# Optimization experiments

Hardware: AMD Instinct MI355X
Metric: run time of the kernel (lower is better)

The kernel has to match this reference:

```python
import jax, jax.numpy as jnp
import numpy as np

N_TYPES = 4
N_REL = 8
N_HEADS = 8
IN_DIM = 256
N_HID = 128
D_K = N_HID // N_HEADS
N_LAYERS = 2
N_NODES = 100000
N_EDGES = 400000


def setup_inputs() -> dict:
    key = jax.random.key(0)
    ks = jax.random.split(key, 24)
    s = 0.05
    inp = {
        'node_feature': jax.random.normal(ks[0], (N_NODES, IN_DIM), jnp.float32),
        'node_type': jax.random.randint(ks[1], (N_NODES,), 0, N_TYPES),
        'edge_index': jax.random.randint(ks[2], (2, N_EDGES), 0, N_NODES),
        'edge_type': jax.random.randint(ks[3], (N_EDGES,), 0, N_REL),
        # per-type input adapters
        'adapt_w': jax.random.normal(ks[4], (N_TYPES, IN_DIM, N_HID), jnp.float32) * s,
        'adapt_b': jnp.zeros((N_TYPES, N_HID), jnp.float32),
        # HGT conv params, stacked over layers
        'k_w': jax.random.normal(ks[5], (N_LAYERS, N_TYPES, N_HID, N_HID), jnp.float32) * s,
        'k_b': jnp.zeros((N_LAYERS, N_TYPES, N_HID), jnp.float32),
        'q_w': jax.random.normal(ks[6], (N_LAYERS, N_TYPES, N_HID, N_HID), jnp.float32) * s,
        'q_b': jnp.zeros((N_LAYERS, N_TYPES, N_HID), jnp.float32),
        'v_w': jax.random.normal(ks[7], (N_LAYERS, N_TYPES, N_HID, N_HID), jnp.float32) * s,
        'v_b': jnp.zeros((N_LAYERS, N_TYPES, N_HID), jnp.float32),
        'a_w': jax.random.normal(ks[8], (N_LAYERS, N_TYPES, N_HID, N_HID), jnp.float32) * s,
        'a_b': jnp.zeros((N_LAYERS, N_TYPES, N_HID), jnp.float32),
        'rel_pri': jnp.ones((N_LAYERS, N_REL, N_HEADS), jnp.float32),
        'rel_att': jnp.tile(jnp.eye(D_K, dtype=jnp.float32), (N_LAYERS, N_REL, N_HEADS, 1, 1))
                   + jax.random.normal(ks[9], (N_LAYERS, N_REL, N_HEADS, D_K, D_K), jnp.float32) * s,
        'rel_msg': jnp.tile(jnp.eye(D_K, dtype=jnp.float32), (N_LAYERS, N_REL, N_HEADS, 1, 1))
                   + jax.random.normal(ks[10], (N_LAYERS, N_REL, N_HEADS, D_K, D_K), jnp.float32) * s,
        'skip': jnp.ones((N_LAYERS, N_TYPES), jnp.float32),
    }
    return inp


def _per_type_linear(x, w, b, node_type, n_idx):
    # x: [N, din], w: [T, din, dout], b: [T, dout] -> gather row for each node's type
    h_all = jnp.einsum('ni,tio->tno', x, w) + b[:, None, :]  # [T, N, dout]
    return h_all[node_type, n_idx]  # [N, dout]


def _edge_softmax(score, tgt, n):
    # score: [E, H]; softmax over incoming edges of each target node
    m = jax.ops.segment_max(score, tgt, num_segments=n)  # [N, H]
    e = jnp.exp(score - m[tgt])
    z = jax.ops.segment_sum(e, tgt, num_segments=n)
    return e / (z[tgt] + 1e-9)


def _hgt_layer(x, node_type, src, tgt, edge_type,
               kw, kb, qw, qb, vw, vb, aw, ab, pri, att_m, msg_m, skip):
    n = x.shape[0]
    n_idx = jnp.arange(n)
    k = _per_type_linear(x, kw, kb, node_type, n_idx).reshape(n, N_HEADS, D_K)
    q = _per_type_linear(x, qw, qb, node_type, n_idx).reshape(n, N_HEADS, D_K)
    v = _per_type_linear(x, vw, vb, node_type, n_idx).reshape(n, N_HEADS, D_K)
    k_src, v_src, q_tgt = k[src], v[src], q[tgt]  # [E, H, dk]
    # per-relation attention/message transforms, accumulated over small fixed R
    k_rel = jnp.zeros_like(k_src)
    v_rel = jnp.zeros_like(v_src)
    for r in range(N_REL):
        msk = (edge_type == r)[:, None, None]
        k_rel = k_rel + jnp.einsum('ehd,hdf->ehf', jnp.where(msk, k_src, 0.0), att_m[r])
        v_rel = v_rel + jnp.einsum('ehd,hdf->ehf', jnp.where(msk, v_src, 0.0), msg_m[r])
    score = (q_tgt * k_rel).sum(-1) * pri[edge_type] * (1.0 / (D_K ** 0.5))  # [E, H]
    att = _edge_softmax(score, tgt, n)
    agg = jax.ops.segment_sum(att[..., None] * v_rel, tgt, num_segments=n)  # [N, H, dk]
    agg = agg.reshape(n, N_HID)
    trans = _per_type_linear(jax.nn.gelu(agg), aw, ab, node_type, n_idx)
    alpha = jax.nn.sigmoid(skip)[node_type][:, None]
    return trans * alpha + x * (1.0 - alpha)


def reference(node_feature, node_type, edge_index, edge_type,
              adapt_w, adapt_b, k_w, k_b, q_w, q_b, v_w, v_b,
              a_w, a_b, rel_pri, rel_att, rel_msg, skip):
    n = node_feature.shape[0]
    n_idx = jnp.arange(n)
    # per-node-type adapter + tanh (gather-linear-scatter, fully vectorized)
    h = jnp.tanh(_per_type_linear(node_feature, adapt_w, adapt_b, node_type, n_idx))
    src, tgt = edge_index[0], edge_index[1]
    for l in range(N_LAYERS):
        h = _hgt_layer(h, node_type, src, tgt, edge_type,
                       k_w[l], k_b[l], q_w[l], q_b[l], v_w[l], v_b[l],
                       a_w[l], a_b[l], rel_pri[l], rel_att[l], rel_msg[l], skip[l])
    return h
```

## Files before the change

### kernel.cpp

```cpp
#include <hip/hip_runtime.h>
#include <hip/hip_fp16.h>
#include <math.h>

constexpr int N_TYPES = 4;
constexpr int N_REL   = 8;
constexpr int N_HEADS = 8;
constexpr int IN_DIM  = 256;
constexpr int N_HID   = 128;
constexpr int D_K     = 16;
constexpr int N_LAYERS= 2;
constexpr int NN      = 100000;
constexpr int NE      = 400000;
constexpr int NBLK    = (NN + 255) / 256;

__device__ __forceinline__ float gelu_f(float x) {
    const float c = 0.7978845608028654f;
    float x3 = x * x * x;
    return 0.5f * x * (1.0f + tanhf(c * (x + 0.044715f * x3)));
}
__device__ __forceinline__ float sigmoid_f(float x) {
    return 1.0f / (1.0f + expf(-x));
}

__global__ __launch_bounds__(256) void count2_kernel(
    const int* __restrict__ ntype, const int* __restrict__ tgt,
    unsigned* ncnt, unsigned* tcnt)
{
    int i = blockIdx.x * 256 + threadIdx.x;
    int lane = threadIdx.x & 63;
    int t = (i < NN) ? ntype[i] : -1;
    #pragma unroll
    for (int tt = 0; tt < N_TYPES; tt++) {
        unsigned long long m = __ballot(t == tt);
        if (m != 0ull && lane == __ffsll((unsigned long long)m) - 1)
            atomicAdd(&ncnt[tt], (unsigned)__popcll(m));
    }
    if (i < NE) atomicAdd(&tcnt[tgt[i]], 1u);
}

__global__ void node_offsets_kernel(unsigned* c)
{
    unsigned a = 0;
    for (int t = 0; t < N_TYPES; t++) { c[8 + t] = a; c[4 + t] = a; a += c[t]; }
    c[8 + N_TYPES] = a;
}

__global__ __launch_bounds__(256) void scan1_kernel(
    const unsigned* __restrict__ cnt, unsigned* __restrict__ eoff,
    unsigned* __restrict__ bsum)
{
    __shared__ unsigned sh[256];
    int i = blockIdx.x * 256 + threadIdx.x;
    unsigned v = (i < NN) ? cnt[i] : 0u;
    sh[threadIdx.x] = v;
    __syncthreads();
    for (int off = 1; off < 256; off <<= 1) {
        unsigned add = (threadIdx.x >= off) ? sh[threadIdx.x - off] : 0u;
        __syncthreads();
        sh[threadIdx.x] += add;
        __syncthreads();
    }
    if (i < NN) eoff[i] = sh[threadIdx.x] - v;
    if (threadIdx.x == 255) bsum[blockIdx.x] = sh[255];
}

__global__ __launch_bounds__(512) void scan2_kernel(unsigned* __restrict__ bsum)
{
    __shared__ unsigned sh[512];
    int i = threadIdx.x;
    unsigned v = (i < NBLK) ? bsum[i] : 0u;
    sh[i] = v;
    __syncthreads();
    for (int off = 1; off < 512; off <<= 1) {
        unsigned add = (i >= off) ? sh[i - off] : 0u;
        __syncthreads();
        sh[i] += add;
        __syncthreads();
    }
    if (i < NBLK) bsum[i] = sh[i] - v;
}

__global__ __launch_bounds__(256) void scan3_kernel(
    unsigned* __restrict__ eoff, const unsigned* __restrict__ bsum,
    unsigned* __restrict__ ecur)
{
    int i = blockIdx.x * 256 + threadIdx.x;
    if (i < NN) {
        unsigned v = eoff[i] + bsum[blockIdx.x];
        eoff[i] = v;
        ecur[i] = v;
    }
    if (i == 0) eoff[NN] = (unsigned)NE;
}

__global__ __launch_bounds__(256) void scatter2_kernel(
    const int* __restrict__ ntype,
    const int* __restrict__ src, const int* __restrict__ tgt,
    const int* __restrict__ etype,
    unsigned* ncur, unsigned* ecur,
    int* __restrict__ nidx,
    int* __restrict__ er_t)
{
    int i = blockIdx.x * 256 + threadIdx.x;
    int lane = threadIdx.x & 63;
    int t = (i < NN) ? ntype[i] : -1;
    #pragma unroll
    for (int tt = 0; tt < N_TYPES; tt++) {
        unsigned long long m = __ballot(t == tt);
        if (m == 0ull) continue;
        int leader = __ffsll((unsigned long long)m) - 1;
        unsigned base = 0;
        if (lane == leader) base = atomicAdd(&ncur[tt], (unsigned)__popcll(m));
        base = __shfl(base, leader, 64);
        if (t == tt) {
            unsigned rank = (unsigned)__popcll(m & ((1ull << lane) - 1ull));
            nidx[base + rank] = i;
        }
    }
    if (i < NE) {
        int tg = tgt[i];
        unsigned p = atomicAdd(&ecur[tg], 1u);
        er_t[p] = (src[i] << 3) | etype[i];
    }
}

template<int DIN, int MIN, int MOUT, int OH>
__global__ __launch_bounds__(256) void ptl128_kernel(
    const float* __restrict__ x,
    const int* __restrict__ nidx,
    const unsigned* __restrict__ noff,
    const float* __restrict__ W,
    const float* __restrict__ Bb,
    const float* __restrict__ skipv,
    const float* __restrict__ hprev,
    void* __restrict__ out)
{
    constexpr int BK = 32;
    const int t = blockIdx.y;
    const unsigned s0 = noff[t], s1 = noff[t + 1];
    const unsigned base = s0 + blockIdx.x * 128u;
    if (base >= s1) return;
    const int nrows = (int)min(128u, s1 - base);

    __shared__ __align__(16) float xs[BK][128];
    __shared__ __align__(16) float wsl[BK][128];
    __shared__ int nid[128];

    const int tid = threadIdx.x;
    if (tid < 128) nid[tid] = nidx[base + (unsigned)min(tid, nrows - 1)];
    __syncthreads();

    const int tx = tid & 15;
    const int ty = tid >> 4;
    const int row = tid & 127, kg = tid >> 7;

    float acc[8][8];
    #pragma unroll
    for (int m = 0; m < 8; m++)
        #pragma unroll
        for (int j = 0; j < 8; j++) acc[m][j] = 0.0f;

    const float* Wt = W + (size_t)t * DIN * 128;

    for (int k0 = 0; k0 < DIN; k0 += BK) {
        {
            const float* xp = x + (size_t)nid[row] * DIN + k0 + kg * 16;
            float4 a0 = ((const float4*)xp)[0];
            float4 a1 = ((const float4*)xp)[1];
            float4 a2 = ((const float4*)xp)[2];
            float4 a3 = ((const float4*)xp)[3];
            float v[16] = {a0.x, a0.y, a0.z, a0.w, a1.x, a1.y, a1.z, a1.w,
                           a2.x, a2.y, a2.z, a2.w, a3.x, a3.y, a3.z, a3.w};
            #pragma unroll
            for (int i = 0; i < 16; i++) {
                float q = v[i];
                if (MIN == 1) q = gelu_f(q);
                xs[kg * 16 + i][row] = q;
            }
        }
        {
            const float* wp = Wt + (size_t)k0 * 128 + tid * 16;
            #pragma unroll
            for (int i = 0; i < 4; i++)
                *(float4*)&wsl[0][tid * 16 + 4 * i] = ((const float4*)wp)[i];
        }
        __syncthreads();
        #pragma unroll 8
        for (int kk = 0; kk < BK; kk++) {
            float4 xa = *(float4*)&xs[kk][ty * 8];
            float4 xb = *(float4*)&xs[kk][ty * 8 + 4];
            float4 wa = *(float4*)&wsl[kk][tx * 8];
            float4 wb = *(float4*)&wsl[kk][tx * 8 + 4];
            float xv[8] = {xa.x, xa.y, xa.z, xa.w, xb.x, xb.y, xb.z, xb.w};
            float wv[8] = {wa.x, wa.y, wa.z, wa.w, wb.x, wb.y, wb.z, wb.w};
            #pragma unroll
            for (int m = 0; m < 8; m++)
                #pragma unroll
                for (int j = 0; j < 8; j++)
                    acc[m][j] += xv[m] * wv[j];
        }
        __syncthreads();
    }

    float alpha = 0.0f;
    if (MOUT == 2) alpha = sigmoid_f(skipv[t]);
    float bb[8];
    #pragma unroll
    for (int j = 0; j < 8; j++) bb[j] = Bb[t * 128 + tx * 8 + j];

    #pragma unroll
    for (int m = 0; m < 8; m++) {
        int rr = ty * 8 + m;
        if (rr < nrows) {
            int n = nid[rr];
            float o[8];
            #pragma unroll
            for (int j = 0; j < 8; j++) o[j] = acc[m][j] + bb[j];
            if (MOUT == 0) {
                #pragma unroll
                for (int j = 0; j < 8; j++) o[j] = tanhf(o[j]);
            } else if (MOUT == 2) {
                const float* hp = hprev + (size_t)n * 128 + tx * 8;
                float4 h0 = *(const float4*)(hp);
                float4 h1 = *(const float4*)(hp + 4);
                float hv[8] = {h0.x, h0.y, h0.z, h0.w, h1.x, h1.y, h1.z, h1.w};
                #pragma unroll
                for (int j = 0; j < 8; j++)
                    o[j] = o[j] * alpha + hv[j] * (1.0f - alpha);
            }
            if (OH == 0) {
                float* op = (float*)out + (size_t)n * 128 + tx * 8;
                *(float4*)(op)     = make_float4(o[0], o[1], o[2], o[3]);
                *(float4*)(op + 4) = make_float4(o[4], o[5], o[6], o[7]);
            } else {
                __align__(16) __half hh[8];
                #pragma unroll
                for (int j = 0; j < 8; j++) hh[j] = __float2half(o[j]);
                __half* op = (__half*)out + (size_t)n * 128 + tx * 8;
                *(uint4*)op = *(uint4*)hh;
            }
        }
    }
}

__global__ __launch_bounds__(256) void hgt_edge_fused(
    const int* __restrict__ er_t,
    const unsigned* __restrict__ eoff,
    const __half* __restrict__ kh,
    const __half* __restrict__ vh,
    const float* __restrict__ att,
    const float* __restrict__ msg,
    const float* __restrict__ pri,
    float* __restrict__ qagg)
{
    __shared__ float aq_lds[2][1024];
    __shared__ float pv_lds[2][1024];
    const int tid  = threadIdx.x;
    const int tsel = tid >> 7;
    const int li   = tid & 127;
    const int h    = li >> 4;
    const int j    = li & 15;
    const int l    = tid & 63;
    const int hb   = tid & 0x30;
    const int t    = blockIdx.x * 2 + tsel;
    if (t >= NN) return;

    const unsigned e0 = eoff[t];
    const unsigned e1 = eoff[t + 1];
    const int deg = (int)(e1 - e0);

    if (deg == 0) {
        qagg[(size_t)t * 128 + li] = 0.0f;
        return;
    }

    float* al = aq_lds[tsel];
    float* pl = pv_lds[tsel];

    #pragma unroll
    for (int r = 0; r < 8; r++) pl[r * 128 + li] = 0.0f;

    const float qo = qagg[(size_t)t * 128 + li];
    float qh[16];
    #pragma unroll
    for (int f = 0; f < 16; f++) qh[f] = __shfl(qo, hb + f, 64);

    int pkl = 0;
    if (l < 16 && e0 + (unsigned)l < e1) pkl = er_t[e0 + l];

    const int dc = min(deg, 16);
    unsigned mask = 0;
    for (int c = 0; c < dc; ++c) mask |= 1u << (__shfl(pkl, c, 64) & 7);
    for (unsigned e = e0 + 16; e < e1; ++e) mask |= 1u << (er_t[e] & 7);

    unsigned need = mask;
    while (need) {
        const int r = __ffs(need) - 1; need &= need - 1;
        const float* Ar = att + (((r * 8 + h) * 16 + j) * 16);
        float4 A0 = ((const float4*)Ar)[0];
        float4 A1 = ((const float4*)Ar)[1];
        float4 A2 = ((const float4*)Ar)[2];
        float4 A3 = ((const float4*)Ar)[3];
        float acc =
            A0.x*qh[0]  + A0.y*qh[1]  + A0.z*qh[2]  + A0.w*qh[3]  +
            A1.x*qh[4]  + A1.y*qh[5]  + A1.z*qh[6]  + A1.w*qh[7]  +
            A2.x*qh[8]  + A2.y*qh[9]  + A2.z*qh[10] + A2.w*qh[11] +
            A3.x*qh[12] + A3.y*qh[13] + A3.z*qh[14] + A3.w*qh[15];
        al[r * 128 + li] = acc * pri[r * 8 + h] * 0.25f;
    }

    float z = 0.0f;
    float* plp = pl + li;
    const float* alp = al + li;
    const __half* kb = kh + li;
    const __half* vb = vh + li;

    unsigned e = e0;
    for (; e + 4 <= e1; e += 4) {
        const int o = (int)(e - e0);
        int p0, p1, p2, p3;
        if (o + 3 < 16) {
            p0 = __shfl(pkl, o + 0, 64);
            p1 = __shfl(pkl, o + 1, 64);
            p2 = __shfl(pkl, o + 2, 64);
            p3 = __shfl(pkl, o + 3, 64);
        } else {
            p0 = er_t[e + 0]; p1 = er_t[e + 1];
            p2 = er_t[e + 2]; p3 = er_t[e + 3];
        }
        const int o0 = (p0 & ~7) << 4;
        const int o1 = (p1 & ~7) << 4;
        const int o2 = (p2 & ~7) << 4;
        const int o3 = (p3 & ~7) << 4;
        const float k0 = __half2float(kb[o0]); const float v0 = __half2float(vb[o0]);
        const float k1 = __half2float(kb[o1]); const float v1 = __half2float(vb[o1]);
        const float k2 = __half2float(kb[o2]); const float v2 = __half2float(vb[o2]);
        const float k3 = __half2float(kb[o3]); const float v3 = __half2float(vb[o3]);
        float s0 = k0 * alp[(p0 & 7) * 128];
        float s1 = k1 * alp[(p1 & 7) * 128];
        float s2 = k2 * alp[(p2 & 7) * 128];
        float s3 = k3 * alp[(p3 & 7) * 128];
        s0 += __shfl_xor(s0, 1); s1 += __shfl_xor(s1, 1);
        s2 += __shfl_xor(s2, 1); s3 += __shfl_xor(s3, 1);
        s0 += __shfl_xor(s0, 2); s1 += __shfl_xor(s1, 2);
        s2 += __shfl_xor(s2, 2); s3 += __shfl_xor(s3, 2);
        s0 += __shfl_xor(s0, 4); s1 += __shfl_xor(s1, 4);
        s2 += __shfl_xor(s2, 4); s3 += __shfl_xor(s3, 4);
        s0 += __shfl_xor(s0, 8); s1 += __shfl_xor(s1, 8);
        s2 += __shfl_xor(s2, 8); s3 += __shfl_xor(s3, 8);
        const float q0 = __expf(s0 - 8.0f);
        const float q1 = __expf(s1 - 8.0f);
        const float q2 = __expf(s2 - 8.0f);
        const float q3 = __expf(s3 - 8.0f);
        z += q0 + q1 + q2 + q3;
        plp[(p0 & 7) * 128] += q0 * v0;
        plp[(p1 & 7) * 128] += q1 * v1;
        plp[(p2 & 7) * 128] += q2 * v2;
        plp[(p3 & 7) * 128] += q3 * v3;
    }
    if (e + 2 <= e1) {
        const int o = (int)(e - e0);
        int p0, p1;
        if (o + 1 < 16) { p0 = __shfl(pkl, o, 64); p1 = __shfl(pkl, o + 1, 64); }
        else            { p0 = er_t[e]; p1 = er_t[e + 1]; }
        const int o0 = (p0 & ~7) << 4;
        const int o1 = (p1 & ~7) << 4;
        const float k0 = __half2float(kb[o0]); const float v0 = __half2float(vb[o0]);
        const float k1 = __half2float(kb[o1]); const float v1 = __half2float(vb[o1]);
        float s0 = k0 * alp[(p0 & 7) * 128];
        float s1 = k1 * alp[(p1 & 7) * 128];
        s0 += __shfl_xor(s0, 1); s1 += __shfl_xor(s1, 1);
        s0 += __shfl_xor(s0, 2); s1 += __shfl_xor(s1, 2);
        s0 += __shfl_xor(s0, 4); s1 += __shfl_xor(s1, 4);
        s0 += __shfl_xor(s0, 8); s1 += __shfl_xor(s1, 8);
        const float q0 = __expf(s0 - 8.0f);
        const float q1 = __expf(s1 - 8.0f);
        z += q0 + q1;
        plp[(p0 & 7) * 128] += q0 * v0;
        plp[(p1 & 7) * 128] += q1 * v1;
        e += 2;
    }
    if (e < e1) {
        const int o = (int)(e - e0);
        const int p0 = (o < 16) ? __shfl(pkl, o, 64) : er_t[e];
        const int o0 = (p0 & ~7) << 4;
        const float k0 = __half2float(kb[o0]); const float v0 = __half2float(vb[o0]);
        float s0 = k0 * alp[(p0 & 7) * 128];
        s0 += __shfl_xor(s0, 1);
        s0 += __shfl_xor(s0, 2);
        s0 += __shfl_xor(s0, 4);
        s0 += __shfl_xor(s0, 8);
        const float q0 = __expf(s0 - 8.0f);
        z += q0;
        plp[(p0 & 7) * 128] += q0 * v0;
    }

    float acc = 0.0f;
    for (int r = 0; r < 8; r++) {
        if (!((mask >> r) & 1)) continue;
        const float* Mr = msg + ((r * 8 + h) * 256) + j;
        const float* sb = pl + r * 128 + h * 16;
        #pragma unroll
        for (int d = 0; d < 16; d++)
            acc += sb[d] * Mr[d * 16];
    }
    qagg[(size_t)t * 128 + li] = acc * __frcp_rn(z + 1e-9f);
}

extern "C" void kernel_launch(void* const* d_in, const int* in_sizes, int n_in,
                              void* d_out, int out_size, void* d_ws, size_t ws_size,
                              hipStream_t stream)
{
    const float* node_feature = (const float*)d_in[0];
    const int*   node_type    = (const int*)d_in[1];
    const int*   edge_index   = (const int*)d_in[2];
    const int*   edge_type    = (const int*)d_in[3];
    const float* adapt_w      = (const float*)d_in[4];
    const float* adapt_b      = (const float*)d_in[5];
    const float* k_w = (const float*)d_in[6];
    const float* k_b = (const float*)d_in[7];
    const float* q_w = (const float*)d_in[8];
    const float* q_b = (const float*)d_in[9];
    const float* v_w = (const float*)d_in[10];
    const float* v_b = (const float*)d_in[11];
    const float* a_w = (const float*)d_in[12];
    const float* a_b = (const float*)d_in[13];
    const float* rel_pri = (const float*)d_in[14];
    const float* rel_att = (const float*)d_in[15];
    const float* rel_msg = (const float*)d_in[16];
    const float* skip    = (const float*)d_in[17];

    const int* src = edge_index;
    const int* tgt = edge_index + NE;

    float* OUT = (float*)d_out;

    char* w = (char*)d_ws;
    auto alloc = [&](size_t bytes) -> void* {
        void* p = (void*)w;
        w += (bytes + 255) & ~(size_t)255;
        return p;
    };
    float*    B0    = (float*)alloc((size_t)NN * 128 * 4);
    float*    B1    = (float*)alloc((size_t)NN * 128 * 4);
    float*    B2    = (float*)alloc((size_t)NN * 128 * 4);
    __half*   KH    = (__half*)alloc((size_t)NN * 128 * 2);
    __half*   VH    = (__half*)alloc((size_t)NN * 128 * 2);
    int*      nidx  = (int*)alloc((size_t)NN * 4);
    int*      er_t  = (int*)alloc((size_t)NE * 4);
    unsigned* tcnt  = (unsigned*)alloc((size_t)NN * 4);
    unsigned* eoff  = (unsigned*)alloc((size_t)(NN + 1) * 4);
    unsigned* ecur  = (unsigned*)alloc((size_t)NN * 4);
    unsigned* bsum  = (unsigned*)alloc((size_t)NBLK * 4);
    unsigned* cnts  = (unsigned*)alloc(16 * 4);

    unsigned* ncnt = cnts;
    unsigned* ncur = cnts + 4;
    unsigned* noff = cnts + 8;

    hipMemsetAsync(cnts, 0, 16 * 4, stream);
    hipMemsetAsync(tcnt, 0, (size_t)NN * 4, stream);

    const int gblocks = (NE + 255) / 256;
    count2_kernel<<<gblocks, 256, 0, stream>>>(node_type, tgt, ncnt, tcnt);
    node_offsets_kernel<<<1, 1, 0, stream>>>(cnts);
    scan1_kernel<<<NBLK, 256, 0, stream>>>(tcnt, eoff, bsum);
    scan2_kernel<<<1, 512, 0, stream>>>(bsum);
    scan3_kernel<<<NBLK, 256, 0, stream>>>(eoff, bsum, ecur);
    scatter2_kernel<<<gblocks, 256, 0, stream>>>(node_type, src, tgt, edge_type,
                                                 ncur, ecur, nidx, er_t);

    dim3 pgrid((NN + 127) / 128, N_TYPES);
    ptl128_kernel<IN_DIM, 0, 0, 0><<<pgrid, 256, 0, stream>>>(
        node_feature, nidx, noff, adapt_w, adapt_b, nullptr, nullptr, B0);

    const int fblocks = (NN + 1) / 2;

    for (int l = 0; l < N_LAYERS; l++) {
        float* hin  = l ? B1 : B0;
        float* qb_  = B2;
        float* hout = l ? OUT : B1;

        const float* kwl = k_w + (size_t)l * N_TYPES * 128 * 128;
        const float* kbl = k_b + (size_t)l * N_TYPES * 128;
        const float* qwl = q_w + (size_t)l * N_TYPES * 128 * 128;
        const float* qbl = q_b + (size_t)l * N_TYPES * 128;
        const float* vwl = v_w + (size_t)l * N_TYPES * 128 * 128;
        const float* vbl = v_b + (size_t)l * N_TYPES * 128;
        const float* awl = a_w + (size_t)l * N_TYPES * 128 * 128;
        const float* abl = a_b + (size_t)l * N_TYPES * 128;
        const float* pril = rel_pri + (size_t)l * N_REL * N_HEADS;
        const float* attl = rel_att + (size_t)l * N_REL * N_HEADS * D_K * D_K;
        const float* msgl = rel_msg + (size_t)l * N_REL * N_HEADS * D_K * D_K;
        const float* skipl = skip + (size_t)l * N_TYPES;

        ptl128_kernel<N_HID, 0, 1, 1><<<pgrid, 256, 0, stream>>>(
            hin, nidx, noff, kwl, kbl, nullptr, nullptr, KH);
        ptl128_kernel<N_HID, 0, 1, 0><<<pgrid, 256, 0, stream>>>(
            hin, nidx, noff, qwl, qbl, nullptr, nullptr, qb_);
        ptl128_kernel<N_HID, 0, 1, 1><<<pgrid, 256, 0, stream>>>(
            hin, nidx, noff, vwl, vbl, nullptr, nullptr, VH);

        hgt_edge_fused<<<fblocks, 256, 0, stream>>>(
            er_t, eoff, KH, VH, attl, msgl, pril, qb_);

        ptl128_kernel<N_HID, 1, 2, 0><<<pgrid, 256, 0, stream>>>(
            qb_, nidx, noff, awl, abl, skipl, hin, hout);
    }
}
```

Measured before the change: 1.198 ms.

## Use fp16 MFMA for per-type linears with fp16 activations throughout

```diff
diff --git a/kernel.cpp b/kernel.cpp
--- a/kernel.cpp
+++ b/kernel.cpp
@@ -13,6 +13,9 @@
 constexpr int NE      = 400000;
 constexpr int NBLK    = (NN + 255) / 256;
 
+typedef _Float16 f16x8 __attribute__((ext_vector_type(8)));
+typedef float    f32x4 __attribute__((ext_vector_type(4)));
+
 __device__ __forceinline__ float gelu_f(float x) {
     const float c = 0.7978845608028654f;
     float x3 = x * x * x;
@@ -124,15 +127,25 @@
     }
 }
 
-template<int DIN, int MIN, int MOUT, int OH>
+__global__ __launch_bounds__(256) void cvt_wT_kernel(
+    const float* __restrict__ W, __half* __restrict__ whT)
+{
+    int gid = blockIdx.x * 256 + threadIdx.x;
+    constexpr int tot = 4 * 128 * 128;
+    if (gid >= tot) return;
+    int t = gid >> 14;
+    int rem = gid & 16383;
+    int k = rem >> 7, n = rem & 127;
+    whT[(((size_t)t * 128 + n) << 7) + k] = __float2half(W[gid]);
+}
+
+template<int DIN, int OH>
 __global__ __launch_bounds__(256) void ptl128_kernel(
     const float* __restrict__ x,
     const int* __restrict__ nidx,
     const unsigned* __restrict__ noff,
     const float* __restrict__ W,
     const float* __restrict__ Bb,
-    const float* __restrict__ skipv,
-    const float* __restrict__ hprev,
     void* __restrict__ out)
 {
     constexpr int BK = 32;
@@ -172,11 +185,7 @@
             float v[16] = {a0.x, a0.y, a0.z, a0.w, a1.x, a1.y, a1.z, a1.w,
                            a2.x, a2.y, a2.z, a2.w, a3.x, a3.y, a3.z, a3.w};
             #pragma unroll
-            for (int i = 0; i < 16; i++) {
-                float q = v[i];
-                if (MIN == 1) q = gelu_f(q);
-                xs[kg * 16 + i][row] = q;
-            }
+            for (int i = 0; i < 16; i++) xs[kg * 16 + i][row] = v[i];
         }
         {
             const float* wp = Wt + (size_t)k0 * 128 + tid * 16;
@@ -202,8 +211,6 @@
         __syncthreads();
     }
 
-    float alpha = 0.0f;
-    if (MOUT == 2) alpha = sigmoid_f(skipv[t]);
     float bb[8];
     #pragma unroll
     for (int j = 0; j < 8; j++) bb[j] = Bb[t * 128 + tx * 8 + j];
@@ -215,19 +222,7 @@
             int n = nid[rr];
             float o[8];
             #pragma unroll
-            for (int j = 0; j < 8; j++) o[j] = acc[m][j] + bb[j];
-            if (MOUT == 0) {
-                #pragma unroll
-                for (int j = 0; j < 8; j++) o[j] = tanhf(o[j]);
-            } else if (MOUT == 2) {
-                const float* hp = hprev + (size_t)n * 128 + tx * 8;
-                float4 h0 = *(const float4*)(hp);
-                float4 h1 = *(const float4*)(hp + 4);
-                float hv[8] = {h0.x, h0.y, h0.z, h0.w, h1.x, h1.y, h1.z, h1.w};
-                #pragma unroll
-                for (int j = 0; j < 8; j++)
-                    o[j] = o[j] * alpha + hv[j] * (1.0f - alpha);
-            }
+            for (int j = 0; j < 8; j++) o[j] = tanhf(acc[m][j] + bb[j]);
             if (OH == 0) {
                 float* op = (float*)out + (size_t)n * 128 + tx * 8;
                 *(float4*)(op)     = make_float4(o[0], o[1], o[2], o[3]);
@@ -243,6 +238,98 @@
     }
 }
 
+template<int MOUT, int OH>
+__global__ __launch_bounds__(256) void mfma_ptl_kernel(
+    const __half* __restrict__ xh,
+    const int* __restrict__ nidx, const unsigned* __restrict__ noff,
+    const __half* __restrict__ whT,
+    const float* __restrict__ Bb,
+    const float* __restrict__ skipv, const __half* __restrict__ hprev,
+    void* __restrict__ out)
+{
+    constexpr int DIN = 128;
+    const int t = blockIdx.y;
+    const unsigned s0 = noff[t], s1 = noff[t + 1];
+    const unsigned base = s0 + blockIdx.x * 128u;
+    if (base >= s1) return;
+    const int nrows = (int)min(128u, s1 - base);
+
+    __shared__ __align__(16) ushort xsh[128][40];
+    __shared__ __align__(16) ushort wsh[128][40];
+    __shared__ int nid[128];
+
+    const int tid = threadIdx.x;
+    if (tid < 128) nid[tid] = nidx[base + (unsigned)min(tid, nrows - 1)];
+    __syncthreads();
+
+    const int lane = tid & 63;
+    const int wave = tid >> 6;
+    const int wr = wave >> 1, wc = wave & 1;
+    const int lm = lane & 15, lk = lane >> 4;
+
+    f32x4 acc[4][4];
+    #pragma unroll
+    for (int a = 0; a < 4; a++)
+        #pragma unroll
+        for (int b = 0; b < 4; b++)
+            acc[a][b] = (f32x4){0.0f, 0.0f, 0.0f, 0.0f};
+
+    const ushort* WT = (const ushort*)(whT + ((size_t)t << 14));
+    const ushort* X  = (const ushort*)xh;
+
+    const int srow = tid & 127, shalf = tid >> 7;
+    const size_t xoff = (size_t)nid[srow] * DIN;
+
+    for (int k0 = 0; k0 < DIN; k0 += 32) {
+        {
+            const ushort* ph = X + xoff + k0 + shalf * 16;
+            *(uint4*)&xsh[srow][shalf * 16]     = *(const uint4*)ph;
+            *(uint4*)&xsh[srow][shalf * 16 + 8] = *(const uint4*)(ph + 8);
+            const ushort* qh = WT + ((size_t)srow << 7) + k0 + shalf * 16;
+            *(uint4*)&wsh[srow][shalf * 16]     = *(const uint4*)qh;
+            *(uint4*)&wsh[srow][shalf * 16 + 8] = *(const uint4*)(qh + 8);
+        }
+        __syncthreads();
+        f16x8 ah[4];
+        #pragma unroll
+        for (int fm = 0; fm < 4; fm++)
+            ah[fm] = *(const f16x8*)&xsh[wr * 64 + fm * 16 + lm][lk * 8];
+        #pragma unroll
+        for (int fn = 0; fn < 4; fn++) {
+            f16x8 bh = *(const f16x8*)&wsh[wc * 64 + fn * 16 + lm][lk * 8];
+            #pragma unroll
+            for (int fm = 0; fm < 4; fm++)
+                acc[fm][fn] = __builtin_amdgcn_mfma_f32_16x16x32_f16(
+                    ah[fm], bh, acc[fm][fn], 0, 0, 0);
+        }
+        __syncthreads();
+    }
+
+    float alpha = 0.0f;
+    if (MOUT == 2) alpha = sigmoid_f(skipv[t]);
+    #pragma unroll
+    for (int fn = 0; fn < 4; fn++) {
+        const int dim = wc * 64 + fn * 16 + lm;
+        const float bias = Bb[t * 128 + dim];
+        #pragma unroll
+        for (int fm = 0; fm < 4; fm++) {
+            #pragma unroll
+            for (int i = 0; i < 4; i++) {
+                int rr = wr * 64 + fm * 16 + lk * 4 + i;
+                if (rr < nrows) {
+                    int n = nid[rr];
+                    float o = acc[fm][fn][i] + bias;
+                    if (MOUT == 2)
+                        o = o * alpha +
+                            __half2float(hprev[(size_t)n * 128 + dim]) * (1.0f - alpha);
+                    if (OH == 0) ((float*)out)[(size_t)n * 128 + dim] = o;
+                    else ((__half*)out)[(size_t)n * 128 + dim] = __float2half(o);
+                }
+            }
+        }
+    }
+}
+
 __global__ __launch_bounds__(256) void hgt_edge_fused(
     const int* __restrict__ er_t,
     const unsigned* __restrict__ eoff,
@@ -251,7 +338,7 @@
     const float* __restrict__ att,
     const float* __restrict__ msg,
     const float* __restrict__ pri,
-    float* __restrict__ qagg)
+    __half* __restrict__ qagg)
 {
     __shared__ float aq_lds[2][1024];
     __shared__ float pv_lds[2][1024];
@@ -270,7 +357,7 @@
     const int deg = (int)(e1 - e0);
 
     if (deg == 0) {
-        qagg[(size_t)t * 128 + li] = 0.0f;
+        qagg[(size_t)t * 128 + li] = __float2half(0.0f);
         return;
     }
 
@@ -280,7 +367,7 @@
     #pragma unroll
     for (int r = 0; r < 8; r++) pl[r * 128 + li] = 0.0f;
 
-    const float qo = qagg[(size_t)t * 128 + li];
+    const float qo = __half2float(qagg[(size_t)t * 128 + li]);
     float qh[16];
     #pragma unroll
     for (int f = 0; f < 16; f++) qh[f] = __shfl(qo, hb + f, 64);
@@ -404,7 +491,8 @@
         for (int d = 0; d < 16; d++)
             acc += sb[d] * Mr[d * 16];
     }
-    qagg[(size_t)t * 128 + li] = acc * __frcp_rn(z + 1e-9f);
+    qagg[(size_t)t * 128 + li] =
+        __float2half(gelu_f(acc * __frcp_rn(z + 1e-9f)));
 }
 
 extern "C" void kernel_launch(void* const* d_in, const int* in_sizes, int n_in,
@@ -441,11 +529,12 @@
         w += (bytes + 255) & ~(size_t)255;
         return p;
     };
-    float*    B0    = (float*)alloc((size_t)NN * 128 * 4);
-    float*    B1    = (float*)alloc((size_t)NN * 128 * 4);
-    float*    B2    = (float*)alloc((size_t)NN * 128 * 4);
+    __half*   H0    = (__half*)alloc((size_t)NN * 128 * 2);
+    __half*   H1    = (__half*)alloc((size_t)NN * 128 * 2);
     __half*   KH    = (__half*)alloc((size_t)NN * 128 * 2);
     __half*   VH    = (__half*)alloc((size_t)NN * 128 * 2);
+    __half*   QA    = (__half*)alloc((size_t)NN * 128 * 2);
+    __half*   WHT   = (__half*)alloc((size_t)8 * 4 * 128 * 128 * 2);
     int*      nidx  = (int*)alloc((size_t)NN * 4);
     int*      er_t  = (int*)alloc((size_t)NE * 4);
     unsigned* tcnt  = (unsigned*)alloc((size_t)NN * 4);
@@ -470,41 +559,56 @@
     scatter2_kernel<<<gblocks, 256, 0, stream>>>(node_type, src, tgt, edge_type,
                                                  ncur, ecur, nidx, er_t);
 
+    {
+        constexpr int wtot = 4 * 128 * 128;
+        const int wblk = (wtot + 255) / 256;
+        const float* Ws[8] = {
+            k_w, q_w, v_w, a_w,
+            k_w + (size_t)wtot, q_w + (size_t)wtot,
+            v_w + (size_t)wtot, a_w + (size_t)wtot };
+        for (int m = 0; m < 8; m++)
+            cvt_wT_kernel<<<wblk, 256, 0, stream>>>(Ws[m], WHT + (size_t)m * wtot);
+    }
+
     dim3 pgrid((NN + 127) / 128, N_TYPES);
-    ptl128_kernel<IN_DIM, 0, 0, 0><<<pgrid, 256, 0, stream>>>(
-        node_feature, nidx, noff, adapt_w, adapt_b, nullptr, nullptr, B0);
+    ptl128_kernel<IN_DIM, 1><<<pgrid, 256, 0, stream>>>(
+        node_feature, nidx, noff, adapt_w, adapt_b, H0);
 
     const int fblocks = (NN + 1) / 2;
+    const size_t wtot = (size_t)4 * 128 * 128;
 
     for (int l = 0; l < N_LAYERS; l++) {
-        float* hin  = l ? B1 : B0;
-        float* qb_  = B2;
-        float* hout = l ? OUT : B1;
-
-        const float* kwl = k_w + (size_t)l * N_TYPES * 128 * 128;
+        __half* hin = l ? H1 : H0;
+
+        const __half* khT = WHT + (size_t)(l * 4 + 0) * wtot;
+        const __half* qhT = WHT + (size_t)(l * 4 + 1) * wtot;
+        const __half* vhT = WHT + (size_t)(l * 4 + 2) * wtot;
+        const __half* ahT = WHT + (size_t)(l * 4 + 3) * wtot;
+
         const float* kbl = k_b + (size_t)l * N_TYPES * 128;
-        const float* qwl = q_w + (size_t)l * N_TYPES * 128 * 128;
         const float* qbl = q_b + (size_t)l * N_TYPES * 128;
-        const float* vwl = v_w + (size_t)l * N_TYPES * 128 * 128;
         const float* vbl = v_b + (size_t)l * N_TYPES * 128;
-        const float* awl = a_w + (size_t)l * N_TYPES * 128 * 128;
         const float* abl = a_b + (size_t)l * N_TYPES * 128;
         const float* pril = rel_pri + (size_t)l * N_REL * N_HEADS;
         const float* attl = rel_att + (size_t)l * N_REL * N_HEADS * D_K * D_K;
         const float* msgl = rel_msg + (size_t)l * N_REL * N_HEADS * D_K * D_K;
         const float* skipl = skip + (size_t)l * N_TYPES;
 
-        ptl128_kernel<N_HID, 0, 1, 1><<<pgrid, 256, 0, stream>>>(
-            hin, nidx, noff, kwl, kbl, nullptr, nullptr, KH);
-        ptl128_kernel<N_HID, 0, 1, 0><<<pgrid, 256, 0, stream>>>(
-            hin, nidx, noff, qwl, qbl, nullptr, nullptr, qb_);
-        ptl128_kernel<N_HID, 0, 1, 1><<<pgrid, 256, 0, stream>>>(
-            hin, nidx, noff, vwl, vbl, nullptr, nullptr, VH);
+        mfma_ptl_kernel<1, 1><<<pgrid, 256, 0, stream>>>(
+            hin, nidx, noff, khT, kbl, nullptr, nullptr, KH);
+        mfma_ptl_kernel<1, 1><<<pgrid, 256, 0, stream>>>(
+            hin, nidx, noff, qhT, qbl, nullptr, nullptr, QA);
+        mfma_ptl_kernel<1, 1><<<pgrid, 256, 0, stream>>>(
+            hin, nidx, noff, vhT, vbl, nullptr, nullptr, VH);
 
         hgt_edge_fused<<<fblocks, 256, 0, stream>>>(
-            er_t, eoff, KH, VH, attl, msgl, pril, qb_);
-
-        ptl128_kernel<N_HID, 1, 2, 0><<<pgrid, 256, 0, stream>>>(
-            qb_, nidx, noff, awl, abl, skipl, hin, hout);
-    }
-}
+            er_t, eoff, KH, VH, attl, msgl, pril, QA);
+
+        if (l == 0)
+            mfma_ptl_kernel<2, 1><<<pgrid, 256, 0, stream>>>(
+                QA, nidx, noff, ahT, abl, skipl, hin, H1);
+        else
+            mfma_ptl_kernel<2, 0><<<pgrid, 256, 0, stream>>>(
+                QA, nidx, noff, ahT, abl, skipl, hin, OUT);
+    }
+}
```

Result: faster. 1.076 ms (-10.2%).
